# Kernel tuning notes

Measured on AMD Instinct MI355X. Metric: run time of the kernel, lower is better.

Reference implementation:

```python
import jax, jax.numpy as jnp
import numpy as np

B, D_IN, H, L, T, OUT = 128, 128, 256, 4, 512, 1

def setup_inputs() -> dict:
    key = jax.random.key(0)
    ks = jax.random.split(key, 16)
    def xavier(k, shape):
        fan_in, fan_out = shape[-1], shape[-2]
        lim = jnp.sqrt(6.0 / (fan_in + fan_out)).astype(jnp.float32)
        return jax.random.uniform(k, shape, jnp.float32, -lim, lim)
    inp = {
        'z': jax.random.normal(ks[0], (B, D_IN), jnp.float32),
        'h0': jax.random.normal(ks[1], (2 * L, B, H), jnp.float32),
        # layer 0 (input size D_IN), [dir, 3H, in]
        'w_ih0': xavier(ks[2], (2, 3 * H, D_IN)),
        'w_hh0': xavier(ks[3], (2, 3 * H, H)),
        'b_ih0': jnp.zeros((2, 3 * H), jnp.float32),
        'b_hh0': jnp.zeros((2, 3 * H), jnp.float32),
        # layers 1..L-1 (input size 2H), [layer, dir, 3H, in]
        'w_ihL': xavier(ks[4], (L - 1, 2, 3 * H, 2 * H)),
        'w_hhL': xavier(ks[5], (L - 1, 2, 3 * H, H)),
        'b_ihL': jnp.zeros((L - 1, 2, 3 * H), jnp.float32),
        'b_hhL': jnp.zeros((L - 1, 2, 3 * H), jnp.float32),
        'fc_w': xavier(ks[6], (OUT, 2 * H)),
        'fc_b': jnp.zeros((OUT,), jnp.float32),
    }
    return inp


def _gru_dir(x, h0, Wih, Whh, bih, bhh, reverse):
    # x: [B,T,in] -> precompute input gates [B,T,3H]
    xg = jnp.einsum('bti,gi->btg', x, Wih) + bih
    if reverse:
        xg = xg[:, ::-1]
    def step(h, xt):  # xt: [B,3H]
        hg = h @ Whh.T + bhh
        xr, xz, xn = jnp.split(xt, 3, axis=-1)
        hr, hz, hn = jnp.split(hg, 3, axis=-1)
        r = jax.nn.sigmoid(xr + hr)
        u = jax.nn.sigmoid(xz + hz)
        n = jnp.tanh(xn + r * hn)
        h_new = (1.0 - u) * n + u * h
        return h_new, h_new
    _, hs = jax.lax.scan(step, h0, jnp.swapaxes(xg, 0, 1))  # [T,B,H]
    hs = jnp.swapaxes(hs, 0, 1)  # [B,T,H]
    return hs[:, ::-1] if reverse else hs


def reference(z, h0, w_ih0, w_hh0, b_ih0, b_hh0, w_ihL, w_hhL, b_ihL, b_hhL, fc_w, fc_b):
    # z [B,D] -> repeated along time [B,T,D]
    x = jnp.broadcast_to(z[:, None, :], (z.shape[0], T, z.shape[1]))
    for l in range(L):
        if l == 0:
            Wf, Wb = w_ih0[0], w_ih0[1]
            Uf, Ub = w_hh0[0], w_hh0[1]
            bif, bib = b_ih0[0], b_ih0[1]
            bhf, bhb = b_hh0[0], b_hh0[1]
        else:
            Wf, Wb = w_ihL[l - 1, 0], w_ihL[l - 1, 1]
            Uf, Ub = w_hhL[l - 1, 0], w_hhL[l - 1, 1]
            bif, bib = b_ihL[l - 1, 0], b_ihL[l - 1, 1]
            bhf, bhb = b_hhL[l - 1, 0], b_hhL[l - 1, 1]
        hf = _gru_dir(x, h0[2 * l], Wf, Uf, bif, bhf, reverse=False)
        hb = _gru_dir(x, h0[2 * l + 1], Wb, Ub, bib, bhb, reverse=True)
        x = jnp.concatenate([hf, hb], axis=-1)  # [B,T,2H]
    # dropout omitted (inference)
    return jnp.tanh(x @ fc_w.T + fc_b)  # [B,T,OUT]
```

## Files before the change

kernel.cpp:

```cpp
#include <hip/hip_runtime.h>
#include <stdint.h>

#define B_   128
#define T_   512
#define H_   256
#define G3_  768
#define D2_  512
#define DIN_ 128
#define M_   (B_*T_)

typedef __attribute__((ext_vector_type(8))) short bf16x8;
typedef __attribute__((ext_vector_type(4))) float f32x4;
typedef unsigned int   u32;
typedef unsigned short u16;

#define MFMA_B16(a,b,c) __builtin_amdgcn_mfma_f32_16x16x32_bf16((a),(b),(c),0,0,0)
#define GLL16(gp, lp) __builtin_amdgcn_global_load_lds( \
    (const __attribute__((address_space(1))) void*)(gp), \
    (__attribute__((address_space(3))) void*)(lp), 16, 0, 0)

__device__ __forceinline__ float bflo(u32 w){
  union { u32 i; float f; } v; v.i = w<<16; return v.f;
}
__device__ __forceinline__ float bfhi(u32 w){
  union { u32 i; float f; } v; v.i = w & 0xffff0000u; return v.f;
}
__device__ __forceinline__ u16 f2bf(float f){
  union { float f; u32 i; } v; v.f = f;
  u32 i = v.i;
  i += 0x7fffu + ((i>>16)&1u);
  return (u16)(i>>16);
}
__device__ __forceinline__ u32 pk2(float a, float b){
  return (u32)f2bf(a) | ((u32)f2bf(b) << 16);
}
__device__ __forceinline__ float sigm(float a){
  float e = __expf(-a);
  return __builtin_amdgcn_rcpf(1.0f + e);
}
__device__ __forceinline__ float tanh_fast(float x){
  float ax = fabsf(x);
  float e  = __expf(-2.0f*ax);
  float th = (1.0f-e)*__builtin_amdgcn_rcpf(1.0f+e);
  return copysignf(th, x);
}


__global__ void sentinel_kernel(float* __restrict__ out, int n, float val){
  int i = blockIdx.x*256 + threadIdx.x;
  if(i < n) out[i] = val;
}

__global__ void pack_bf16(const float* __restrict__ src, u16* __restrict__ dst, int n){
  int i = blockIdx.x*256 + threadIdx.x;
  if(i < n) dst[i] = f2bf(src[i]);
}

__global__ void pack_whh(const float* __restrict__ s0, const float* __restrict__ s1,
                         int n0, int n1, u16* __restrict__ dst){
  int i = blockIdx.x*256 + threadIdx.x;
  if(i < n0) dst[i] = f2bf(s0[i]);
  else if(i < n0+n1) dst[i] = f2bf(s1[i-n0]);
}

__global__ void xg0_kernel(const float* __restrict__ z, const float* __restrict__ w,
                           const float* __restrict__ bih, const float* __restrict__ bhh,
                           float* __restrict__ out)
{
  int idx = blockIdx.x*256 + threadIdx.x;
  int g = idx % G3_;
  int b = (idx / G3_) & (B_-1);
  int d = idx / (G3_*B_);
  const float* zr = z + b*DIN_;
  const float* wr = w + (size_t)(d*G3_ + g)*DIN_;
  float acc = bih[d*G3_ + g];
  if(g < D2_) acc += bhh[d*G3_ + g];
#pragma unroll 4
  for(int k=0;k<DIN_;++k) acc += zr[k]*wr[k];
  out[idx] = acc;
}

__global__ __launch_bounds__(256,1) void gemm_xg(
    const u16* __restrict__ A,
    const u16* __restrict__ W,
    const float* __restrict__ bih,
    const float* __restrict__ bhh,
    u16* __restrict__ out)
{
  const int virt = (blockIdx.x & 7)*768 + (blockIdx.x >> 3);
  const int nt  = virt % 6;
  const int mt  = (virt/6) & 511;
  const int dir = virt / (6*512);
  const int m0 = mt*128, n0 = nt*128;
  const int tid = threadIdx.x, lane = tid & 63, w = tid >> 6;
  const u16* Wd = W + (size_t)dir*G3_*512;

  __shared__ alignas(16) u16 lds[2][2][128*64];

  const int wr = w>>1, wc = w&1;

  auto stage = [&](int buf, int kb){
    const u16* Ab = A  + (size_t)m0*512 + kb*64;
    const u16* Bb = Wd + (size_t)n0*512 + kb*64;
#pragma unroll
    for(int q=0;q<4;++q){
      int c = q*256 + tid;
      int row = c>>3, c8 = c&7;
      GLL16(Ab + (size_t)row*512 + c8*8, &lds[buf][0][(q*256 + w*64)*8]);
      GLL16(Bb + (size_t)row*512 + c8*8, &lds[buf][1][(q*256 + w*64)*8]);
    }
  };

  f32x4 acc[4][4];
#pragma unroll
  for(int a=0;a<4;++a)
#pragma unroll
  for(int b=0;b<4;++b) acc[a][b] = (f32x4){0.f,0.f,0.f,0.f};

  stage(0,0);
  for(int kb=0;kb<8;++kb){
    __syncthreads();
    if(kb<7) stage((kb+1)&1, kb+1);
    const int buf = kb&1;
#pragma unroll
    for(int ks=0;ks<2;++ks){
      bf16x8 afr[4], bfr[4];
#pragma unroll
      for(int mi=0;mi<4;++mi)
        afr[mi] = *(const bf16x8*)&lds[buf][0][(wr*64+mi*16+(lane&15))*64 + ks*32 + (lane>>4)*8];
#pragma unroll
      for(int ni=0;ni<4;++ni)
        bfr[ni] = *(const bf16x8*)&lds[buf][1][(wc*64+ni*16+(lane&15))*64 + ks*32 + (lane>>4)*8];
#pragma unroll
      for(int mi=0;mi<4;++mi)
#pragma unroll
      for(int ni=0;ni<4;++ni)
        acc[mi][ni] = MFMA_B16(afr[mi], bfr[ni], acc[mi][ni]);
    }
  }

#pragma unroll
  for(int mi=0;mi<4;++mi)
#pragma unroll
  for(int ni=0;ni<4;++ni)
#pragma unroll
  for(int r=0;r<4;++r){
    int row = m0 + wr*64 + mi*16 + (lane>>4)*4 + r;
    int col = n0 + wc*64 + ni*16 + (lane&15);
    float bb = bih[dir*G3_ + col];
    if(col < D2_) bb += bhh[dir*G3_ + col];
    float v = acc[mi][ni][r] + bb;
    out[(size_t)dir*M_*G3_ + (size_t)row*G3_ + col] = f2bf(v);
  }
}

template<int XGF32>
__global__ __launch_bounds__(512,2) void gru_scan(
    const u16* __restrict__ whh2,
    const float* __restrict__ bhh2,
    const float* __restrict__ h02,
    const void* __restrict__ xg_all,
    size_t dirStride, size_t strideB, size_t strideT,
    u16* __restrict__ xout)
{
  const int blk = blockIdx.x & 7;
  const int dir = blockIdx.x >> 3;
  const int tid = threadIdx.x;
  const int lane = tid & 63;
  const int w   = tid >> 6;
  const int l4  = lane & 15;
  const int lg  = lane >> 4;
  const int b0  = blk*16;
  const int colw = w*32;
  const int ES  = XGF32 ? 4 : 2;

  const u16*  Whh = whh2 + (size_t)dir*G3_*H_;
  const float* H0 = h02  + (size_t)dir*B_*H_;
  const char* XGb = (const char*)xg_all + (size_t)dir*dirStride*ES;
  char* XOb = (char*)xout;

  __shared__ alignas(16) char smem[147456];
  char* wlds  = smem;
  char* hbase = smem + 114688;

  bf16x8 Wf[2][2][8];
#pragma unroll
  for(int g=0; g<2; ++g)
#pragma unroll
  for(int i=0; i<2; ++i)
#pragma unroll
  for(int kt=0; kt<8; ++kt)
    Wf[g][i][kt] = *(const bf16x8*)(Whh + (size_t)(g*H_ + colw + i*16 + l4)*H_ + kt*32 + lg*8);

  bf16x8 wn7[2];
#pragma unroll
  for(int i=0; i<2; ++i){
#pragma unroll
    for(int kt=0; kt<7; ++kt){
      const u16* gp = Whh + (size_t)(2*H_ + colw + i*16 + l4)*H_ + kt*32 + lg*8;
      GLL16(gp, wlds + (((w*2+i)*7+kt)<<10));
    }
    wn7[i] = *(const bf16x8*)(Whh + (size_t)(2*H_ + colw + i*16 + l4)*H_ + 7*32 + lg*8);
  }

  f32x4 bn4[2];
#pragma unroll
  for(int i=0;i<2;++i)
    bn4[i] = *(const f32x4*)(bhh2 + dir*G3_ + 2*H_ + colw + i*16 + lg*4);

  f32x4 hown[2];
  u32 hwa[2];
#pragma unroll
  for(int i=0;i<2;++i){
    hown[i] = *(const f32x4*)(H0 + (size_t)(b0+l4)*H_ + colw + i*16 + lg*4);
    hwa[i]  = (u32)(l4*512 + (colw + i*16 + lg*4)*2) ^ (u32)((l4&7)<<4);
    u32 h0p = pk2(hown[i][0], hown[i][1]);
    u32 h1p = pk2(hown[i][2], hown[i][3]);
    u32 l0p = pk2(hown[i][0]-bflo(h0p), hown[i][1]-bfhi(h0p));
    u32 l1p = pk2(hown[i][2]-bflo(h1p), hown[i][3]-bfhi(h1p));
    *(uint2*)(hbase + hwa[i])        = make_uint2(h0p, h1p);
    *(uint2*)(hbase + 8192 + hwa[i]) = make_uint2(l0p, l1p);
  }

  const int t0 = dir ? (T_-1) : 0;
  u32 xbase[2], obase[2];
#pragma unroll
  for(int i=0;i<2;++i){
    xbase[i] = (u32)(((size_t)(b0+l4)*strideB + colw + i*16 + lg*4) * ES);
    obase[i] = (u32)(((((size_t)(b0+l4))*T_)*D2_ + dir*H_ + colw + i*16 + lg*4)*2);
  }
  u32 tXB = (u32)((size_t)t0*strideT*ES);
  const int dXg = dir ? -(int)(strideT*ES) : (int)(strideT*ES);
  u32 tOB = (u32)(t0*D2_*2);
  const int dOut = dir ? -(D2_*2) : (D2_*2);

  f32x4 xgv[2][3];
#pragma unroll
  for(int i=0;i<2;++i)
#pragma unroll
  for(int g=0;g<3;++g){
    if(XGF32){
      xgv[i][g] = *(const f32x4*)(XGb + xbase[i] + tXB + g*(H_*4));
    } else {
      uint2 p = *(const uint2*)(XGb + xbase[i] + tXB + g*(H_*2));
      xgv[i][g] = (f32x4){bflo(p.x), bfhi(p.x), bflo(p.y), bfhi(p.y)};
    }
  }

  __syncthreads();

  for(int s=0; s<T_; ++s){
    const char* hc = hbase + ((s&1)<<14);
    char*       hx = hbase + (((s+1)&1)<<14);
    const u32 tXBn = tXB + (u32)dXg;
    const bool pre = (strideT != 0) && (s+1 < T_);

    f32x4 ar[2], az[2], an[2];
#pragma unroll
    for(int i=0;i<2;++i){
      ar[i] = (f32x4){0.f,0.f,0.f,0.f};
      az[i] = (f32x4){0.f,0.f,0.f,0.f};
      an[i] = bn4[i];
    }
#pragma unroll
    for(int kt=0; kt<8; ++kt){
      u32 aao = ((u32)(l4*512 + kt*64 + lg*16)) ^ (u32)((l4&7)<<4);
      bf16x8 ah = *(const bf16x8*)(hc + aao);
      bf16x8 al = *(const bf16x8*)(hc + 8192 + aao);
#pragma unroll
      for(int i=0;i<2;++i){
        bf16x8 wn = (kt<7) ? *(const bf16x8*)(wlds + ((((w*2+i)*7+kt)<<10) + lane*16))
                           : wn7[i];
        ar[i] = MFMA_B16(Wf[0][i][kt], ah, ar[i]);
        az[i] = MFMA_B16(Wf[1][i][kt], ah, az[i]);
        an[i] = MFMA_B16(wn, ah, an[i]);
        an[i] = MFMA_B16(wn, al, an[i]);
      }
    }

#pragma unroll
    for(int i=0;i<2;++i){
      f32x4 hnew;
#pragma unroll
      for(int r=0;r<4;++r){
        float rg = sigm(xgv[i][0][r] + ar[i][r]);
        float ug = sigm(xgv[i][1][r] + az[i][r]);
        float ng = tanh_fast(xgv[i][2][r] + rg*an[i][r]);
        float h  = hown[i][r];
        hnew[r]  = ng + ug*(h - ng);
      }
      hown[i] = hnew;
      u32 h0p = pk2(hnew[0], hnew[1]);
      u32 h1p = pk2(hnew[2], hnew[3]);
      u32 l0p = pk2(hnew[0]-bflo(h0p), hnew[1]-bfhi(h0p));
      u32 l1p = pk2(hnew[2]-bflo(h1p), hnew[3]-bfhi(h1p));
      *(uint2*)(hx + hwa[i])        = make_uint2(h0p, h1p);
      *(uint2*)(hx + 8192 + hwa[i]) = make_uint2(l0p, l1p);
      *(uint2*)(XOb + obase[i] + tOB) = make_uint2(h0p, h1p);
      if(pre){
#pragma unroll
        for(int g=0;g<3;++g){
          if(XGF32){
            xgv[i][g] = *(const f32x4*)(XGb + xbase[i] + tXBn + g*(H_*4));
          } else {
            uint2 p = *(const uint2*)(XGb + xbase[i] + tXBn + g*(H_*2));
            xgv[i][g] = (f32x4){bflo(p.x), bfhi(p.x), bflo(p.y), bfhi(p.y)};
          }
        }
      }
    }
    tXB = tXBn;
    tOB += (u32)dOut;
    __syncthreads();
  }
}

__global__ __launch_bounds__(256,1) void fc_kernel(
    const u16* __restrict__ x, const float* __restrict__ fcw,
    const float* __restrict__ fcb, float* __restrict__ out)
{
  int gw = (blockIdx.x*256 + threadIdx.x) >> 6;
  int lane = threadIdx.x & 63;
  const u16* xr = x + (size_t)gw*D2_ + lane*8;
  bf16x8 v = *(const bf16x8*)xr;
  float s = 0.f;
#pragma unroll
  for(int e=0;e<8;++e) s += bflo((u32)(u16)v[e]) * fcw[lane*8+e];
#pragma unroll
  for(int off=32; off>0; off>>=1) s += __shfl_down(s, off, 64);
  if(lane==0) out[gw] = tanh_fast(s + fcb[0]);
}

extern "C" void kernel_launch(void* const* d_in, const int* in_sizes, int n_in,
                              void* d_out, int out_size, void* d_ws, size_t ws_size,
                              hipStream_t stream)
{
  const float* z     = (const float*)d_in[0];
  const float* h0    = (const float*)d_in[1];
  const float* w_ih0 = (const float*)d_in[2];
  const float* w_hh0 = (const float*)d_in[3];
  const float* b_ih0 = (const float*)d_in[4];
  const float* b_hh0 = (const float*)d_in[5];
  const float* w_ihL = (const float*)d_in[6];
  const float* w_hhL = (const float*)d_in[7];
  const float* b_ihL = (const float*)d_in[8];
  const float* b_hhL = (const float*)d_in[9];
  const float* fc_w  = (const float*)d_in[10];
  const float* fc_b  = (const float*)d_in[11];
  float* outp = (float*)d_out;

  const size_t sz_xg = (size_t)2*M_*G3_*2;
  const size_t sz_X  = (size_t)M_*D2_*2;
  if(ws_size < sz_xg + sz_X){
    float val = 1024.0f + (float)(ws_size >> 20);
    sentinel_kernel<<<(out_size+255)/256, 256, 0, stream>>>(outp, out_size, val);
    return;
  }
  u16* xg = (u16*)d_ws;
  u16* X  = (u16*)((char*)d_ws + sz_xg);
  float* xg0 = (float*)d_ws;

  u16* whh_tmp = (u16*)X;
  u16* wpack   = (u16*)d_in[7];
  u16* whh_bf  = (u16*)d_in[6];

  const int nhh0 = 2*G3_*H_;
  const int nhhL = 3*2*G3_*H_;
  const int nwih = 3*2*G3_*512;
  pack_whh<<<(nhh0+nhhL+255)/256, 256, 0, stream>>>(w_hh0, w_hhL, nhh0, nhhL, whh_tmp);
  pack_bf16<<<(nwih+255)/256, 256, 0, stream>>>(w_ihL, wpack, nwih);
  hipMemcpyAsync(whh_bf, whh_tmp, (size_t)(nhh0+nhhL)*2, hipMemcpyDeviceToDevice, stream);
  xg0_kernel<<<(2*B_*G3_)/256, 256, 0, stream>>>(z, w_ih0, b_ih0, b_hh0, xg0);

  gru_scan<1><<<16, 512, 0, stream>>>(whh_bf, b_hh0, h0, xg0,
      (size_t)B_*G3_, (size_t)G3_, (size_t)0, X);

  for(int l=1; l<4; ++l){
    const u16* wih = wpack + (size_t)(l-1)*2*G3_*512;
    const float* bi = b_ihL + (size_t)(l-1)*2*G3_;
    const float* bh = b_hhL + (size_t)(l-1)*2*G3_;
    gemm_xg<<<2*512*6, 256, 0, stream>>>(X, wih, bi, bh, xg);
    const u16* whl = whh_bf + (size_t)l*2*G3_*H_;
    const float* h0l = h0 + (size_t)2*l*B_*H_;
    gru_scan<0><<<16, 512, 0, stream>>>(whl, bh, h0l, xg,
        (size_t)M_*G3_, (size_t)T_*G3_, (size_t)G3_, X);
  }

  fc_kernel<<<(B_*T_)/4, 256, 0, stream>>>(X, fc_w, fc_b, outp);
}
```

Before: 6.440 ms.

## Drop split-bf16 hidden-state precision and hold all recurrent weights in registers

The GRU scan no longer stores a low-order bf16 residual of h for the n-gate matmul. It holds all three gate weight blocks in registers instead of streaming the n-gate weights from LDS, and the LDS shrinks to a small double-buffered h tile. The layer-0 input gates are now stored as bf16 rather than fp32, tanh uses a branchless formula, and the per-step __syncthreads is replaced by a raw LDS waitcnt plus s_barrier. The aim is to cut per-step MFMA count and LDS traffic on the serial recurrence, at the cost of lower numerical accuracy and higher register pressure (possible spills with 512 threads).

```diff
diff --git a/kernel.cpp b/kernel.cpp
--- a/kernel.cpp
+++ b/kernel.cpp
@@ -39,10 +39,8 @@
   return __builtin_amdgcn_rcpf(1.0f + e);
 }
 __device__ __forceinline__ float tanh_fast(float x){
-  float ax = fabsf(x);
-  float e  = __expf(-2.0f*ax);
-  float th = (1.0f-e)*__builtin_amdgcn_rcpf(1.0f+e);
-  return copysignf(th, x);
+  float e = __expf(-2.0f*x);
+  return __builtin_fmaf(2.0f, __builtin_amdgcn_rcpf(1.0f + e), -1.0f);
 }
 
 
@@ -65,7 +63,7 @@
 
 __global__ void xg0_kernel(const float* __restrict__ z, const float* __restrict__ w,
                            const float* __restrict__ bih, const float* __restrict__ bhh,
-                           float* __restrict__ out)
+                           u16* __restrict__ out)
 {
   int idx = blockIdx.x*256 + threadIdx.x;
   int g = idx % G3_;
@@ -77,7 +75,7 @@
   if(g < D2_) acc += bhh[d*G3_ + g];
 #pragma unroll 4
   for(int k=0;k<DIN_;++k) acc += zr[k]*wr[k];
-  out[idx] = acc;
+  out[idx] = f2bf(acc);
 }
 
 __global__ __launch_bounds__(256,1) void gemm_xg(
@@ -154,12 +152,12 @@
   }
 }
 
-template<int XGF32>
+template<int TINV>
 __global__ __launch_bounds__(512,2) void gru_scan(
     const u16* __restrict__ whh2,
     const float* __restrict__ bhh2,
     const float* __restrict__ h02,
-    const void* __restrict__ xg_all,
+    const u16* __restrict__ xg_all,
     size_t dirStride, size_t strideB, size_t strideT,
     u16* __restrict__ xout)
 {
@@ -172,35 +170,23 @@
   const int lg  = lane >> 4;
   const int b0  = blk*16;
   const int colw = w*32;
-  const int ES  = XGF32 ? 4 : 2;
 
   const u16*  Whh = whh2 + (size_t)dir*G3_*H_;
   const float* H0 = h02  + (size_t)dir*B_*H_;
-  const char* XGb = (const char*)xg_all + (size_t)dir*dirStride*ES;
+  const char* XGb = (const char*)(xg_all + (size_t)dir*dirStride);
   char* XOb = (char*)xout;
 
-  __shared__ alignas(16) char smem[147456];
-  char* wlds  = smem;
-  char* hbase = smem + 114688;
-
-  bf16x8 Wf[2][2][8];
-#pragma unroll
-  for(int g=0; g<2; ++g)
+  __shared__ alignas(16) char hbase[16384];
+
+  bf16x8 Wf[3][2][8];
+#pragma unroll
+  for(int g=0; g<3; ++g)
 #pragma unroll
   for(int i=0; i<2; ++i)
 #pragma unroll
-  for(int kt=0; kt<8; ++kt)
+  for(int kt=0; kt<8; ++kt){
     Wf[g][i][kt] = *(const bf16x8*)(Whh + (size_t)(g*H_ + colw + i*16 + l4)*H_ + kt*32 + lg*8);
-
-  bf16x8 wn7[2];
-#pragma unroll
-  for(int i=0; i<2; ++i){
-#pragma unroll
-    for(int kt=0; kt<7; ++kt){
-      const u16* gp = Whh + (size_t)(2*H_ + colw + i*16 + l4)*H_ + kt*32 + lg*8;
-      GLL16(gp, wlds + (((w*2+i)*7+kt)<<10));
-    }
-    wn7[i] = *(const bf16x8*)(Whh + (size_t)(2*H_ + colw + i*16 + l4)*H_ + 7*32 + lg*8);
+    asm volatile("" : "+v"(Wf[g][i][kt]));
   }
 
   f32x4 bn4[2];
@@ -214,46 +200,35 @@
   for(int i=0;i<2;++i){
     hown[i] = *(const f32x4*)(H0 + (size_t)(b0+l4)*H_ + colw + i*16 + lg*4);
     hwa[i]  = (u32)(l4*512 + (colw + i*16 + lg*4)*2) ^ (u32)((l4&7)<<4);
-    u32 h0p = pk2(hown[i][0], hown[i][1]);
-    u32 h1p = pk2(hown[i][2], hown[i][3]);
-    u32 l0p = pk2(hown[i][0]-bflo(h0p), hown[i][1]-bfhi(h0p));
-    u32 l1p = pk2(hown[i][2]-bflo(h1p), hown[i][3]-bfhi(h1p));
-    *(uint2*)(hbase + hwa[i])        = make_uint2(h0p, h1p);
-    *(uint2*)(hbase + 8192 + hwa[i]) = make_uint2(l0p, l1p);
+    *(uint2*)(hbase + hwa[i]) = make_uint2(pk2(hown[i][0], hown[i][1]),
+                                           pk2(hown[i][2], hown[i][3]));
   }
 
   const int t0 = dir ? (T_-1) : 0;
   u32 xbase[2], obase[2];
 #pragma unroll
   for(int i=0;i<2;++i){
-    xbase[i] = (u32)(((size_t)(b0+l4)*strideB + colw + i*16 + lg*4) * ES);
+    xbase[i] = (u32)(((size_t)(b0+l4)*strideB + colw + i*16 + lg*4) * 2);
     obase[i] = (u32)(((((size_t)(b0+l4))*T_)*D2_ + dir*H_ + colw + i*16 + lg*4)*2);
   }
-  u32 tXB = (u32)((size_t)t0*strideT*ES);
-  const int dXg = dir ? -(int)(strideT*ES) : (int)(strideT*ES);
+  u32 tXB = (u32)((size_t)t0*strideT*2);
+  const int dXg = dir ? -(int)(strideT*2) : (int)(strideT*2);
   u32 tOB = (u32)(t0*D2_*2);
   const int dOut = dir ? -(D2_*2) : (D2_*2);
 
-  f32x4 xgv[2][3];
+  uint2 xgv[2][3];
 #pragma unroll
   for(int i=0;i<2;++i)
 #pragma unroll
-  for(int g=0;g<3;++g){
-    if(XGF32){
-      xgv[i][g] = *(const f32x4*)(XGb + xbase[i] + tXB + g*(H_*4));
-    } else {
-      uint2 p = *(const uint2*)(XGb + xbase[i] + tXB + g*(H_*2));
-      xgv[i][g] = (f32x4){bflo(p.x), bfhi(p.x), bflo(p.y), bfhi(p.y)};
-    }
-  }
+  for(int g=0;g<3;++g)
+    xgv[i][g] = *(const uint2*)(XGb + xbase[i] + tXB + g*(H_*2));
 
   __syncthreads();
 
   for(int s=0; s<T_; ++s){
-    const char* hc = hbase + ((s&1)<<14);
-    char*       hx = hbase + (((s+1)&1)<<14);
+    const char* hc = hbase + ((s&1)<<13);
+    char*       hx = hbase + (((s+1)&1)<<13);
     const u32 tXBn = tXB + (u32)dXg;
-    const bool pre = (strideT != 0) && (s+1 < T_);
 
     f32x4 ar[2], az[2], an[2];
 #pragma unroll
@@ -266,52 +241,47 @@
     for(int kt=0; kt<8; ++kt){
       u32 aao = ((u32)(l4*512 + kt*64 + lg*16)) ^ (u32)((l4&7)<<4);
       bf16x8 ah = *(const bf16x8*)(hc + aao);
-      bf16x8 al = *(const bf16x8*)(hc + 8192 + aao);
 #pragma unroll
       for(int i=0;i<2;++i){
-        bf16x8 wn = (kt<7) ? *(const bf16x8*)(wlds + ((((w*2+i)*7+kt)<<10) + lane*16))
-                           : wn7[i];
         ar[i] = MFMA_B16(Wf[0][i][kt], ah, ar[i]);
         az[i] = MFMA_B16(Wf[1][i][kt], ah, az[i]);
-        an[i] = MFMA_B16(wn, ah, an[i]);
-        an[i] = MFMA_B16(wn, al, an[i]);
+        an[i] = MFMA_B16(Wf[2][i][kt], ah, an[i]);
       }
     }
 
 #pragma unroll
     for(int i=0;i<2;++i){
+      f32x4 xrv = (f32x4){bflo(xgv[i][0].x), bfhi(xgv[i][0].x),
+                          bflo(xgv[i][0].y), bfhi(xgv[i][0].y)};
+      f32x4 xzv = (f32x4){bflo(xgv[i][1].x), bfhi(xgv[i][1].x),
+                          bflo(xgv[i][1].y), bfhi(xgv[i][1].y)};
+      f32x4 xnv = (f32x4){bflo(xgv[i][2].x), bfhi(xgv[i][2].x),
+                          bflo(xgv[i][2].y), bfhi(xgv[i][2].y)};
       f32x4 hnew;
 #pragma unroll
       for(int r=0;r<4;++r){
-        float rg = sigm(xgv[i][0][r] + ar[i][r]);
-        float ug = sigm(xgv[i][1][r] + az[i][r]);
-        float ng = tanh_fast(xgv[i][2][r] + rg*an[i][r]);
+        float rg = sigm(xrv[r] + ar[i][r]);
+        float ug = sigm(xzv[r] + az[i][r]);
+        float ng = tanh_fast(xnv[r] + rg*an[i][r]);
         float h  = hown[i][r];
         hnew[r]  = ng + ug*(h - ng);
       }
       hown[i] = hnew;
-      u32 h0p = pk2(hnew[0], hnew[1]);
-      u32 h1p = pk2(hnew[2], hnew[3]);
-      u32 l0p = pk2(hnew[0]-bflo(h0p), hnew[1]-bfhi(h0p));
-      u32 l1p = pk2(hnew[2]-bflo(h1p), hnew[3]-bfhi(h1p));
-      *(uint2*)(hx + hwa[i])        = make_uint2(h0p, h1p);
-      *(uint2*)(hx + 8192 + hwa[i]) = make_uint2(l0p, l1p);
-      *(uint2*)(XOb + obase[i] + tOB) = make_uint2(h0p, h1p);
-      if(pre){
-#pragma unroll
-        for(int g=0;g<3;++g){
-          if(XGF32){
-            xgv[i][g] = *(const f32x4*)(XGb + xbase[i] + tXBn + g*(H_*4));
-          } else {
-            uint2 p = *(const uint2*)(XGb + xbase[i] + tXBn + g*(H_*2));
-            xgv[i][g] = (f32x4){bflo(p.x), bfhi(p.x), bflo(p.y), bfhi(p.y)};
-          }
-        }
+      uint2 hp = make_uint2(pk2(hnew[0], hnew[1]), pk2(hnew[2], hnew[3]));
+      *(uint2*)(hx + hwa[i]) = hp;
+      *(uint2*)(XOb + obase[i] + tOB) = hp;
+      if(!TINV && s+1 < T_){
+#pragma unroll
+        for(int g=0;g<3;++g)
+          xgv[i][g] = *(const uint2*)(XGb + xbase[i] + tXBn + g*(H_*2));
       }
     }
     tXB = tXBn;
     tOB += (u32)dOut;
-    __syncthreads();
+
+    asm volatile("s_waitcnt lgkmcnt(0)" ::: "memory");
+    __builtin_amdgcn_s_barrier();
+    __builtin_amdgcn_sched_barrier(0);
   }
 }
 
@@ -358,7 +328,7 @@
   }
   u16* xg = (u16*)d_ws;
   u16* X  = (u16*)((char*)d_ws + sz_xg);
-  float* xg0 = (float*)d_ws;
+  u16* xg0 = (u16*)d_ws;
 
   u16* whh_tmp = (u16*)X;
   u16* wpack   = (u16*)d_in[7];
```

New measurement: 6.632 ms. +3.0%, slower.
